# Kernel optimization log

Hardware: AMD Instinct MI355X
Metric: run time of the kernel (lower is better)

The kernel has to match this reference:

```python
import jax, jax.numpy as jnp
import numpy as np

B, T, D, EXP, K = 4, 2048, 1024, 2, 4
H = D * EXP


def setup_inputs() -> dict:
    key = jax.random.key(0)
    ks = jax.random.split(key, 8)
    x = jax.random.normal(ks[0], (B, T, D), jnp.float32)
    W_in = jax.random.normal(ks[1], (2 * H, D), jnp.float32) * D ** -0.5
    s_conv = 1.0 / np.sqrt(K)  # fan_in = (in_ch/groups)*K = K
    W_conv = jax.random.uniform(ks[2], (H, 1, K), jnp.float32, -s_conv, s_conv)
    b_conv = jax.random.uniform(ks[3], (H,), jnp.float32, -s_conv, s_conv)
    W_gates = jax.random.normal(ks[4], (3 * H, H), jnp.float32) * H ** -0.5
    s_g = 1.0 / np.sqrt(H)
    b_gates = jax.random.uniform(ks[5], (3 * H,), jnp.float32, -s_g, s_g)
    W_out = jax.random.normal(ks[6], (D, H), jnp.float32) * H ** -0.5
    alpha_p = jnp.asarray(1.0, jnp.float32)
    return {"x": x, "W_in": W_in, "W_conv": W_conv, "b_conv": b_conv,
            "W_gates": W_gates, "b_gates": b_gates, "W_out": W_out,
            "alpha_p": alpha_p}


def _scan_combine(c1, c2):
    a1, b1 = c1
    a2, b2 = c2
    return (a1 * a2, a2 * b1 + b2)


def reference(x, W_in, W_conv, b_conv, W_gates, b_gates, W_out, alpha_p):
    # input projection -> gate branch and conv branch, each [B,T,H]
    gi = jnp.einsum('btd,ed->bte', x, W_in)
    gate, u = jnp.split(gi, 2, axis=-1)
    # causal depthwise conv over time (torch pads K-1 both sides then keeps [:T])
    uc = jnp.transpose(u, (0, 2, 1))  # [B,H,T]
    v = jax.lax.conv_general_dilated(
        uc, W_conv, window_strides=(1,), padding=[(K - 1, 0)],
        dimension_numbers=('NCH', 'OIH', 'NCH'), feature_group_count=H)
    v = jnp.transpose(v + b_conv[None, :, None], (0, 2, 1))  # [B,T,H]
    # gates
    g = jnp.einsum('bth,gh->btg', v, W_gates) + b_gates
    f, i, o = jnp.split(g, 3, axis=-1)
    # reversed_sigmoid=True: alpha = sigmoid(-f) ** relu(alpha_p)
    alpha = jax.nn.sigmoid(-f) ** jax.nn.relu(alpha_p)
    xin = jax.nn.sigmoid(i) * v
    # diagonal linear recurrence h_t = alpha_t * h_{t-1} + xin_t via parallel scan
    _, h = jax.lax.associative_scan(_scan_combine, (alpha, xin), axis=1)
    h = jax.nn.sigmoid(o) * h
    return jnp.einsum('bth,dh->btd', jax.nn.gelu(gate, approximate=False) * h, W_out)
```

## Files before the change

### kernel.cpp

```cpp
#include <hip/hip_runtime.h>
#include <hip/hip_bf16.h>
#include <cstdint>
#include <cstddef>

#define B_ 4
#define T_ 2048
#define D_ 1024
#define H_ 2048

typedef __attribute__((ext_vector_type(8))) short s8v;
typedef __attribute__((ext_vector_type(4))) float f4v;

__device__ __forceinline__ float bflo(unsigned int u){ union{unsigned int i;float f;}c; c.i=u<<16; return c.f; }
__device__ __forceinline__ float bfhi(unsigned int u){ union{unsigned int i;float f;}c; c.i=u&0xffff0000u; return c.f; }
__device__ __forceinline__ unsigned short f2bf(float f){
    __hip_bfloat16 h = __float2bfloat16(f);
    union { __hip_bfloat16 h; unsigned short u; } c; c.h = h; return c.u;
}
__device__ __forceinline__ unsigned int pk2(float lo, float hi){
    return (unsigned int)f2bf(lo) | ((unsigned int)f2bf(hi) << 16);
}
__device__ __forceinline__ float sigm(float x){ return 1.f/(1.f+expf(-x)); }

__device__ __forceinline__ void gload16(const void* g, void* l){
    __builtin_amdgcn_global_load_lds(
        (const __attribute__((address_space(1))) unsigned int*)g,
        (__attribute__((address_space(3))) unsigned int*)l, 16, 0, 0);
}

__global__ __launch_bounds__(256)
void cvt8(const float* __restrict__ s, unsigned short* __restrict__ d)
{
    size_t i = ((size_t)blockIdx.x*256 + threadIdx.x)*8;
    float4 a = *(const float4*)(s+i), b = *(const float4*)(s+i+4);
    uint4 o; o.x=pk2(a.x,a.y); o.y=pk2(a.z,a.w); o.z=pk2(b.x,b.y); o.w=pk2(b.z,b.w);
    *(uint4*)(d+i)=o;
}

template<int EPI>
__global__ __launch_bounds__(512)
void mgemm256(const unsigned short* __restrict__ A, int lda,
              const unsigned short* __restrict__ Bw, int K, int N,
              const float* __restrict__ bias,
              unsigned short* __restrict__ C0, unsigned short* __restrict__ C1,
              unsigned short* __restrict__ C2,
              const unsigned short* __restrict__ vsrc, const float* __restrict__ app)
{
    __shared__ unsigned short As[2][256*64];
    __shared__ unsigned short Bs[2][256*64];
    const int tid = threadIdx.x;
    const int lane = tid & 63;
    const int wid = tid >> 6;
    const int wm = wid >> 2;
    const int wn = wid & 3;

    const int nxb = N >> 8;
    const int nwg = nxb * 32;
    const int orig = blockIdx.x;
    const int q = nwg >> 3;
    const int wg = (orig & 7) * q + (orig >> 3);
    const int m0 = (wg & 31) * 256;
    const int n0 = (wg >> 5) * 256;

    const int srow_in8 = lane >> 3;
    const int sslot    = (lane & 7) ^ srow_in8;
    const int NT = K >> 6;

    const int fr = lane & 15, fg = lane >> 4;
    const int sw = fr & 7;
    int aoff[8][2], boff[4][2];
#pragma unroll
    for (int m = 0; m < 8; ++m) {
        int row = wm*128 + m*16 + fr;
#pragma unroll
        for (int s = 0; s < 2; ++s)
            aoff[m][s] = row*128 + (((s*4 + fg) ^ sw) * 16);
    }
#pragma unroll
    for (int n = 0; n < 4; ++n) {
        int row = wn*64 + n*16 + fr;
#pragma unroll
        for (int s = 0; s < 2; ++s)
            boff[n][s] = row*128 + (((s*4 + fg) ^ sw) * 16);
    }

    f4v acc[8][4];
#pragma unroll
    for (int m = 0; m < 8; ++m)
#pragma unroll
        for (int n = 0; n < 4; ++n) { f4v z4 = {0.f,0.f,0.f,0.f}; acc[m][n] = z4; }

    auto stageA = [&](int pp, int kt) {
#pragma unroll
        for (int c = 0; c < 4; ++c) {
            int row = c*64 + wid*8 + srow_in8;
            gload16(A + (size_t)(m0 + row)*lda + kt*64 + sslot*8,
                    (void*)&As[pp][(c*64 + wid*8) * 64]);
        }
    };
    auto stageB = [&](int pp, int kt) {
#pragma unroll
        for (int c = 0; c < 4; ++c) {
            int row = c*64 + wid*8 + srow_in8;
            gload16(Bw + (size_t)(n0 + row)*K + kt*64 + sslot*8,
                    (void*)&Bs[pp][(c*64 + wid*8) * 64]);
        }
    };

    stageA(0, 0);
    stageB(0, 0);
    __syncthreads();

    for (int t = 0; t < NT; ++t) {
        const int p = t & 1;
        const char* Asb = (const char*)&As[p][0];
        const char* Bsb = (const char*)&Bs[p][0];
        const bool more = (t + 1 < NT);
#pragma unroll
        for (int ph = 0; ph < 4; ++ph) {
            const int mh = ph >> 1, nh = ph & 1;
            s8v a[4][2], b[2][2];
#pragma unroll
            for (int mi = 0; mi < 4; ++mi)
#pragma unroll
                for (int s = 0; s < 2; ++s)
                    a[mi][s] = *(const s8v*)(Asb + aoff[mh*4 + mi][s]);
#pragma unroll
            for (int ni = 0; ni < 2; ++ni)
#pragma unroll
                for (int s = 0; s < 2; ++s)
                    b[ni][s] = *(const s8v*)(Bsb + boff[nh*2 + ni][s]);
            if (ph == 0 && more) stageA(p ^ 1, t + 1);
            if (ph == 1 && more) stageB(p ^ 1, t + 1);
            __builtin_amdgcn_s_setprio(1);
#pragma unroll
            for (int mi = 0; mi < 4; ++mi)
#pragma unroll
                for (int ni = 0; ni < 2; ++ni)
#pragma unroll
                    for (int s = 0; s < 2; ++s)
                        acc[mh*4+mi][nh*2+ni] = __builtin_amdgcn_mfma_f32_16x16x32_bf16(
                            a[mi][s], b[ni][s], acc[mh*4+mi][nh*2+ni], 0, 0, 0);
            __builtin_amdgcn_s_setprio(0);
        }
        __syncthreads();
    }

    float apv = 1.f; bool ap1 = true;
    if (EPI == 2) { apv = fmaxf(app[0], 0.f); ap1 = (apv == 1.0f); }
    const int cr = (lane >> 4) * 4;
    const int cc = lane & 15;
#pragma unroll
    for (int m = 0; m < 8; ++m) {
        const int grow0 = m0 + wm*128 + m*16 + cr;
#pragma unroll
        for (int n = 0; n < 4; ++n) {
            const int colb = n0 + wn*64 + n*16;
            const int gcol = colb + cc;
            if (EPI == 1) {
                unsigned short* dst = (colb < H_) ? C0 : C1;
                const int pc = gcol & (H_-1);
#pragma unroll
                for (int j = 0; j < 4; ++j)
                    dst[(size_t)(grow0+j)*H_ + pc] = f2bf(acc[m][n][j]);
            } else {
                const int plane = colb >> 11;
                const int pc = gcol & (H_-1);
#pragma unroll
                for (int j = 0; j < 4; ++j) {
                    float val = acc[m][n][j] + bias[gcol];
                    const size_t off = (size_t)(grow0+j)*H_ + pc;
                    if (plane == 0) {
                        float s = 1.f/(1.f+expf(val));
                        C0[off] = f2bf(ap1 ? s : powf(s, apv));
                    } else if (plane == 1) {
                        C1[off] = f2bf(sigm(val) * bflo(vsrc[off]));
                    } else {
                        C2[off] = f2bf(sigm(val));
                    }
                }
            }
        }
    }
}

template<int AM, int BM, int EPI>
__global__ __launch_bounds__(256)
void mgemm(const void* __restrict__ Asrc, int lda,
           const void* __restrict__ Bsrc, int K, int N,
           const float* __restrict__ bias,
           unsigned short* __restrict__ C0, unsigned short* __restrict__ C1,
           unsigned short* __restrict__ C2, float* __restrict__ Cf,
           const unsigned short* __restrict__ vsrc, const float* __restrict__ app)
{
    __shared__ unsigned short As[128*64];
    __shared__ unsigned short Bs[128*64];
    const int tid = threadIdx.x;
    const int lane = tid & 63;
    const int wid = tid >> 6;

    const int nwg = gridDim.x * 64;
    const int orig = blockIdx.y * gridDim.x + blockIdx.x;
    const int q = nwg >> 3;
    const int wg = (orig & 7) * q + (orig >> 3);
    const int m0 = (wg & 63) * 128;
    const int n0 = (wg >> 6) * 128;

    const int ar0 = wid * 32;
    const int alr = lane >> 3;
    const int alj = lane & 7;
    const int rr = tid >> 1;
    const int kh = tid & 1;

    const int wm = wid >> 1, wn = wid & 1;
    const int fr = lane & 15, fg = lane >> 4;
    int aoff[4][2], boff[4][2];
#pragma unroll
    for (int m = 0; m < 4; ++m) {
        int row = wm*64 + m*16 + fr;
#pragma unroll
        for (int s = 0; s < 2; ++s)
            aoff[m][s] = row*128 + (((s*4 + fg) ^ (row & 7)) * 16);
    }
#pragma unroll
    for (int n = 0; n < 4; ++n) {
        int row = wn*64 + n*16 + fr;
#pragma unroll
        for (int s = 0; s < 2; ++s)
            boff[n][s] = row*128 + (((s*4 + fg) ^ (row & 7)) * 16);
    }
    const char* Asc = (const char*)As;
    const char* Bsc = (const char*)Bs;

    f4v acc[4][4];
#pragma unroll
    for (int m = 0; m < 4; ++m)
#pragma unroll
        for (int n = 0; n < 4; ++n) { f4v z4 = {0.f,0.f,0.f,0.f}; acc[m][n] = z4; }

    for (int k0 = 0; k0 < K; k0 += 64) {
        if (AM == 1) {
            const unsigned short* Ab = (const unsigned short*)Asrc;
#pragma unroll
            for (int i = 0; i < 4; ++i) {
                int row = ar0 + i*8 + alr;
                int ss = alj ^ alr;
                const char* g = (const char*)(Ab + (size_t)(m0+row)*lda + k0) + ss*16;
                gload16(g, (void*)((char*)As + (ar0 + i*8)*128));
            }
        } else {
            const float* src = (const float*)Asrc + (size_t)(m0+rr)*lda + k0 + kh*32;
            float4 v[8];
#pragma unroll
            for (int i = 0; i < 8; ++i) v[i] = ((const float4*)src)[i];
#pragma unroll
            for (int qd = 0; qd < 4; ++qd) {
                uint4 w;
                w.x = pk2(v[2*qd].x, v[2*qd].y);   w.y = pk2(v[2*qd].z, v[2*qd].w);
                w.z = pk2(v[2*qd+1].x, v[2*qd+1].y); w.w = pk2(v[2*qd+1].z, v[2*qd+1].w);
                int j = (kh*4 + qd) ^ (rr & 7);
                *(uint4*)((char*)As + rr*128 + j*16) = w;
            }
        }
        if (BM == 1) {
            const unsigned short* Bb = (const unsigned short*)Bsrc;
#pragma unroll
            for (int i = 0; i < 4; ++i) {
                int row = ar0 + i*8 + alr;
                int ss = alj ^ alr;
                const char* g = (const char*)(Bb + (size_t)(n0+row)*K + k0) + ss*16;
                gload16(g, (void*)((char*)Bs + (ar0 + i*8)*128));
            }
        } else {
            const float* src = (const float*)Bsrc + (size_t)(n0+rr)*K + k0 + kh*32;
            float4 v[8];
#pragma unroll
            for (int i = 0; i < 8; ++i) v[i] = ((const float4*)src)[i];
#pragma unroll
            for (int qd = 0; qd < 4; ++qd) {
                uint4 w;
                w.x = pk2(v[2*qd].x, v[2*qd].y);   w.y = pk2(v[2*qd].z, v[2*qd].w);
                w.z = pk2(v[2*qd+1].x, v[2*qd+1].y); w.w = pk2(v[2*qd+1].z, v[2*qd+1].w);
                int j = (kh*4 + qd) ^ (rr & 7);
                *(uint4*)((char*)Bs + rr*128 + j*16) = w;
            }
        }
        __syncthreads();
#pragma unroll
        for (int s = 0; s < 2; ++s) {
            s8v a[4], b[4];
#pragma unroll
            for (int m = 0; m < 4; ++m) a[m] = *(const s8v*)(Asc + aoff[m][s]);
#pragma unroll
            for (int n = 0; n < 4; ++n) b[n] = *(const s8v*)(Bsc + boff[n][s]);
#pragma unroll
            for (int m = 0; m < 4; ++m)
#pragma unroll
                for (int n = 0; n < 4; ++n)
                    acc[m][n] = __builtin_amdgcn_mfma_f32_16x16x32_bf16(a[m], b[n], acc[m][n], 0, 0, 0);
        }
        __syncthreads();
    }

    float apv = 1.f; bool ap1 = true;
    if (EPI == 2) { apv = fmaxf(app[0], 0.f); ap1 = (apv == 1.0f); }
    const int cr = (lane >> 4) * 4;
    const int cc = lane & 15;
#pragma unroll
    for (int m = 0; m < 4; ++m) {
        const int grow0 = m0 + wm*64 + m*16 + cr;
#pragma unroll
        for (int n = 0; n < 4; ++n) {
            const int colb = n0 + wn*64 + n*16;
            const int gcol = colb + cc;
            if (EPI == 0) {
#pragma unroll
                for (int j = 0; j < 4; ++j)
                    Cf[(size_t)(grow0+j)*N + gcol] = acc[m][n][j];
            } else if (EPI == 1) {
                unsigned short* dst = (colb < H_) ? C0 : C1;
                const int pc = gcol & (H_-1);
#pragma unroll
                for (int j = 0; j < 4; ++j)
                    dst[(size_t)(grow0+j)*H_ + pc] = f2bf(acc[m][n][j]);
            } else {
                const int plane = colb >> 11;
                const int pc = gcol & (H_-1);
#pragma unroll
                for (int j = 0; j < 4; ++j) {
                    float val = acc[m][n][j] + bias[gcol];
                    const size_t off = (size_t)(grow0+j)*H_ + pc;
                    if (plane == 0) {
                        float s = 1.f/(1.f+expf(val));
                        C0[off] = f2bf(ap1 ? s : powf(s, apv));
                    } else if (plane == 1) {
                        C1[off] = f2bf(sigm(val) * bflo(vsrc[off]));
                    } else {
                        C2[off] = f2bf(sigm(val));
                    }
                }
            }
        }
    }
}

__global__ __launch_bounds__(256)
void conv8(const unsigned short* __restrict__ u, const float* __restrict__ Wc,
           const float* __restrict__ bc, unsigned short* __restrict__ v)
{
    size_t i8 = ((size_t)blockIdx.x*256 + threadIdx.x) * 8;
    int h = (int)(i8 % H_);
    size_t bt = i8 / H_;
    int t = (int)(bt % T_);
    float w[8][4], acc[8];
#pragma unroll
    for (int j = 0; j < 8; ++j) {
        float4 wr = *(const float4*)(Wc + (h+j)*4);
        w[j][0]=wr.x; w[j][1]=wr.y; w[j][2]=wr.z; w[j][3]=wr.w;
        acc[j] = bc[h+j];
    }
    const unsigned short* up = u + bt*H_ + h;
#pragma unroll
    for (int k = 0; k < 4; ++k) {
        int dt = 3 - k;
        if (t >= dt) {
            uint4 r = *(const uint4*)(up - (size_t)dt*H_);
            float e[8] = {bflo(r.x),bfhi(r.x),bflo(r.y),bfhi(r.y),
                          bflo(r.z),bfhi(r.z),bflo(r.w),bfhi(r.w)};
#pragma unroll
            for (int j = 0; j < 8; ++j) acc[j] = fmaf(e[j], w[j][k], acc[j]);
        }
    }
    uint4 o;
    o.x = pk2(acc[0],acc[1]); o.y = pk2(acc[2],acc[3]);
    o.z = pk2(acc[4],acc[5]); o.w = pk2(acc[6],acc[7]);
    *(uint4*)(v + i8) = o;
}

__global__ __launch_bounds__(256)
void scan_chunk8(const unsigned short* __restrict__ al, const unsigned short* __restrict__ xi,
                 float* __restrict__ cA, float* __restrict__ cB, int CT)
{
    int hh = threadIdx.x * 8;
    int c = blockIdx.y, b = blockIdx.z;
    size_t base = ((size_t)b*T_ + (size_t)c*CT)*H_ + hh;
    float A[8], Bv[8];
#pragma unroll
    for (int j=0;j<8;++j){ A[j]=1.f; Bv[j]=0.f; }
    for (int t = 0; t < CT; ++t) {
        uint4 wa = *(const uint4*)(al+base);
        uint4 wx = *(const uint4*)(xi+base);
        float a[8]={bflo(wa.x),bfhi(wa.x),bflo(wa.y),bfhi(wa.y),bflo(wa.z),bfhi(wa.z),bflo(wa.w),bfhi(wa.w)};
        float x[8]={bflo(wx.x),bfhi(wx.x),bflo(wx.y),bfhi(wx.y),bflo(wx.z),bfhi(wx.z),bflo(wx.w),bfhi(wx.w)};
#pragma unroll
        for (int j=0;j<8;++j){ A[j]*=a[j]; Bv[j]=fmaf(a[j],Bv[j],x[j]); }
        base += H_;
    }
    size_t ci = ((size_t)b*gridDim.y + c)*H_ + hh;
    *(float4*)(cA+ci)   = (float4){A[0],A[1],A[2],A[3]};
    *(float4*)(cA+ci+4) = (float4){A[4],A[5],A[6],A[7]};
    *(float4*)(cB+ci)   = (float4){Bv[0],Bv[1],Bv[2],Bv[3]};
    *(float4*)(cB+ci+4) = (float4){Bv[4],Bv[5],Bv[6],Bv[7]};
}

__global__ __launch_bounds__(256)
void scan_carry8(const float* __restrict__ cA, const float* __restrict__ cB,
                 float* __restrict__ cin, int NC)
{
    int gt = blockIdx.x*256 + threadIdx.x;
    int hh = (gt * 8) % H_;
    int b  = (gt * 8) / H_;
    float h[8];
#pragma unroll
    for (int j=0;j<8;++j) h[j]=0.f;
    for (int c = 0; c < NC; ++c) {
        size_t ci = ((size_t)b*NC + c)*H_ + hh;
        *(float4*)(cin+ci)   = (float4){h[0],h[1],h[2],h[3]};
        *(float4*)(cin+ci+4) = (float4){h[4],h[5],h[6],h[7]};
        float4 a0 = *(const float4*)(cA+ci), a1 = *(const float4*)(cA+ci+4);
        float4 b0 = *(const float4*)(cB+ci), b1 = *(const float4*)(cB+ci+4);
        float a[8]={a0.x,a0.y,a0.z,a0.w,a1.x,a1.y,a1.z,a1.w};
        float x[8]={b0.x,b0.y,b0.z,b0.w,b1.x,b1.y,b1.z,b1.w};
#pragma unroll
        for (int j=0;j<8;++j) h[j] = fmaf(a[j], h[j], x[j]);
    }
}

__global__ __launch_bounds__(256)
void scan_apply8(const unsigned short* __restrict__ al, const unsigned short* __restrict__ xi,
                 const unsigned short* __restrict__ so, const unsigned short* __restrict__ ga,
                 const float* __restrict__ cin, unsigned short* __restrict__ z, int CT)
{
    int hh = threadIdx.x * 8;
    int c = blockIdx.y, b = blockIdx.z;
    size_t base = ((size_t)b*T_ + (size_t)c*CT)*H_ + hh;
    size_t ci = ((size_t)b*gridDim.y + c)*H_ + hh;
    float h[8];
    {
        float4 h0 = *(const float4*)(cin+ci), h1 = *(const float4*)(cin+ci+4);
        h[0]=h0.x; h[1]=h0.y; h[2]=h0.z; h[3]=h0.w;
        h[4]=h1.x; h[5]=h1.y; h[6]=h1.z; h[7]=h1.w;
    }
    for (int t = 0; t < CT; ++t) {
        uint4 wa = *(const uint4*)(al+base);
        uint4 wx = *(const uint4*)(xi+base);
        uint4 ws_ = *(const uint4*)(so+base);
        uint4 wg = *(const uint4*)(ga+base);
        float a[8]={bflo(wa.x),bfhi(wa.x),bflo(wa.y),bfhi(wa.y),bflo(wa.z),bfhi(wa.z),bflo(wa.w),bfhi(wa.w)};
        float x[8]={bflo(wx.x),bfhi(wx.x),bflo(wx.y),bfhi(wx.y),bflo(wx.z),bfhi(wx.z),bflo(wx.w),bfhi(wx.w)};
        float s[8]={bflo(ws_.x),bfhi(ws_.x),bflo(ws_.y),bfhi(ws_.y),bflo(ws_.z),bfhi(ws_.z),bflo(ws_.w),bfhi(ws_.w)};
        float g[8]={bflo(wg.x),bfhi(wg.x),bflo(wg.y),bfhi(wg.y),bflo(wg.z),bfhi(wg.z),bflo(wg.w),bfhi(wg.w)};
        float zo[8];
#pragma unroll
        for (int j=0;j<8;++j) {
            h[j] = fmaf(a[j], h[j], x[j]);
            float ge = 0.5f*g[j]*(1.f+erff(g[j]*0.70710678118654752f));
            zo[j] = ge * s[j] * h[j];
        }
        uint4 o;
        o.x = pk2(zo[0],zo[1]); o.y = pk2(zo[2],zo[3]);
        o.z = pk2(zo[4],zo[5]); o.w = pk2(zo[6],zo[7]);
        *(uint4*)(z + base) = o;
        base += H_;
    }
}

__global__ void zero_out(float* __restrict__ out, size_t n)
{
    for (size_t i = (size_t)blockIdx.x*256 + threadIdx.x; i < n; i += (size_t)gridDim.x*256)
        out[i] = 0.f;
}

extern "C" void kernel_launch(void* const* d_in, const int* in_sizes, int n_in,
                              void* d_out, int out_size, void* d_ws, size_t ws_size,
                              hipStream_t stream)
{
    const float* x       = (const float*)d_in[0];
    const float* W_in    = (const float*)d_in[1];
    const float* W_conv  = (const float*)d_in[2];
    const float* b_conv  = (const float*)d_in[3];
    const float* W_gates = (const float*)d_in[4];
    const float* b_gates = (const float*)d_in[5];
    const float* W_out   = (const float*)d_in[6];
    const float* alpha_p = (const float*)d_in[7];
    float* out = (float*)d_out;

    const size_t plane = (size_t)B_ * T_ * H_;
    unsigned short* gate = (unsigned short*)d_ws;
    unsigned short* u    = gate + plane;
    unsigned short* v    = u + plane;
    unsigned short* xin  = v + plane;
    unsigned short* so   = xin + plane;
    char* R = (char*)(so + plane);

    const size_t x_elems  = (size_t)B_*T_*D_;
    const size_t wg_elems = (size_t)3*H_*H_;
    const size_t wi_elems = (size_t)2*H_*D_;
    const size_t wo_elems = (size_t)D_*H_;
    const int NCF = 64;
    const size_t carry_b = 3*(size_t)B_*NCF*H_*4;
    const size_t Rneed = x_elems*2 > carry_b + wo_elems*2 ? x_elems*2 : carry_b + wo_elems*2;
    const size_t need_fast = 5*plane*2 + Rneed;

    if (ws_size >= need_fast && (size_t)out_size*4 >= (wg_elems + wi_elems)*2) {
        unsigned short* wgb  = (unsigned short*)d_out;
        unsigned short* winb = wgb + wg_elems;
        unsigned short* xb   = (unsigned short*)R;
        float* cAp  = (float*)R;
        float* cBp  = cAp + (size_t)B_*NCF*H_;
        float* cinp = cBp + (size_t)B_*NCF*H_;
        unsigned short* woutb = (unsigned short*)(cinp + (size_t)B_*NCF*H_);
        const int CT = T_ / NCF;

        cvt8<<<(unsigned)(x_elems/2048),  256, 0, stream>>>(x, xb);
        cvt8<<<(unsigned)(wi_elems/2048), 256, 0, stream>>>(W_in, winb);
        cvt8<<<(unsigned)(wg_elems/2048), 256, 0, stream>>>(W_gates, wgb);
        mgemm256<1><<<dim3(16*32), 512, 0, stream>>>(
            xb, D_, winb, D_, 2*H_, nullptr, gate, u, nullptr, nullptr, nullptr);
        conv8<<<(unsigned)(plane/8/256), 256, 0, stream>>>(u, W_conv, b_conv, v);
        cvt8<<<(unsigned)(wo_elems/2048), 256, 0, stream>>>(W_out, woutb);
        mgemm256<2><<<dim3(24*32), 512, 0, stream>>>(
            v, H_, wgb, H_, 3*H_, b_gates, u, xin, so, v, alpha_p);
        scan_chunk8<<<dim3(1,NCF,B_), 256, 0, stream>>>(u, xin, cAp, cBp, CT);
        scan_carry8<<<(B_*H_/8)/256, 256, 0, stream>>>(cAp, cBp, cinp, NCF);
        scan_apply8<<<dim3(1,NCF,B_), 256, 0, stream>>>(u, xin, so, gate, cinp, v, CT);
        mgemm<1,1,0><<<dim3(8,64), 256, 0, stream>>>(
            v, H_, woutb, H_, D_, nullptr, nullptr, nullptr, nullptr, out, nullptr, nullptr);
        return;
    }

    float* cAp = (float*)R;
    int NC = 64;
    if (ws_size < 5*plane*2 + 3*(size_t)B_*64*H_*4) {
        NC = 16;
        if (ws_size < 5*plane*2 + 3*(size_t)B_*16*H_*4) {
            zero_out<<<2048, 256, 0, stream>>>(out, (size_t)out_size);
            return;
        }
    }
    const int CT = T_ / NC;
    float* cBp  = cAp + (size_t)B_*NC*H_;
    float* cinp = cBp + (size_t)B_*NC*H_;

    mgemm<0,0,1><<<dim3(32,64), 256, 0, stream>>>(
        x, D_, W_in, D_, 2*H_, nullptr, gate, u, nullptr, nullptr, nullptr, nullptr);
    conv8<<<(unsigned)(plane/8/256), 256, 0, stream>>>(u, W_conv, b_conv, v);
    mgemm<1,0,2><<<dim3(48,64), 256, 0, stream>>>(
        v, H_, W_gates, H_, 3*H_, b_gates, u, xin, so, nullptr, v, alpha_p);
    scan_chunk8<<<dim3(1,NC,B_), 256, 0, stream>>>(u, xin, cAp, cBp, CT);
    scan_carry8<<<(B_*H_/8)/256, 256, 0, stream>>>(cAp, cBp, cinp, NC);
    scan_apply8<<<dim3(1,NC,B_), 256, 0, stream>>>(u, xin, so, gate, cinp, v, CT);
    mgemm<1,0,0><<<dim3(8,64), 256, 0, stream>>>(
        v, H_, W_out, H_, D_, nullptr, nullptr, nullptr, nullptr, out, nullptr, nullptr);
}
```

Measured before the change: 643.3 us.

## Rework 256x256 GEMM into 4-stage K=32 pipeline with one barrier per step

Replaces the double-buffered K=64 tile GEMM with a four-deep ring of K=32 LDS tiles. Tiles are prefetched three steps ahead, and explicit vmcnt waits plus a single barrier per iteration replace the per-phase staging and __syncthreads. The LDS layout and swizzle change to pack row pairs, and launch bounds now request two blocks per CU. The goal is to hide global-load latency better and cut synchronisation. The trade-off is more loop iterations with less MFMA work each, plus hand-tuned waitcnt logic that is fragile.

```diff
diff --git a/kernel.cpp b/kernel.cpp
--- a/kernel.cpp
+++ b/kernel.cpp
@@ -38,50 +38,57 @@
 }
 
 template<int EPI>
-__global__ __launch_bounds__(512)
-void mgemm256(const unsigned short* __restrict__ A, int lda,
-              const unsigned short* __restrict__ Bw, int K, int N,
-              const float* __restrict__ bias,
-              unsigned short* __restrict__ C0, unsigned short* __restrict__ C1,
-              unsigned short* __restrict__ C2,
-              const unsigned short* __restrict__ vsrc, const float* __restrict__ app)
-{
-    __shared__ unsigned short As[2][256*64];
-    __shared__ unsigned short Bs[2][256*64];
+__global__ __launch_bounds__(512, 2)
+void pgemm(const unsigned short* __restrict__ A, int lda,
+           const unsigned short* __restrict__ Bw, int K, int N,
+           const float* __restrict__ bias,
+           unsigned short* __restrict__ C0, unsigned short* __restrict__ C1,
+           unsigned short* __restrict__ C2,
+           const unsigned short* __restrict__ vsrc, const float* __restrict__ app)
+{
+    __shared__ unsigned short lds[4][16384];
     const int tid = threadIdx.x;
     const int lane = tid & 63;
     const int wid = tid >> 6;
     const int wm = wid >> 2;
     const int wn = wid & 3;
 
-    const int nxb = N >> 8;
-    const int nwg = nxb * 32;
+    const int nwg = (N >> 8) * 32;
     const int orig = blockIdx.x;
     const int q = nwg >> 3;
     const int wg = (orig & 7) * q + (orig >> 3);
     const int m0 = (wg & 31) * 256;
     const int n0 = (wg >> 5) * 256;
 
-    const int srow_in8 = lane >> 3;
-    const int sslot    = (lane & 7) ^ srow_in8;
-    const int NT = K >> 6;
+    const char* srcA[2]; const char* srcB[2];
+    int dstOff[2];
+#pragma unroll
+    for (int r = 0; r < 2; ++r) {
+        int si = r*512 + tid;
+        int rp = si >> 3;
+        int sl = (si & 7) ^ (rp & 7);
+        int row = 2*rp + (sl >> 2);
+        int fg  = sl & 3;
+        srcA[r] = (const char*)(A  + (size_t)(m0 + row) * lda + fg*8);
+        srcB[r] = (const char*)(Bw + (size_t)(n0 + row) * K   + fg*8);
+        dstOff[r] = (r*512 + wid*64) * 16;
+    }
 
     const int fr = lane & 15, fg = lane >> 4;
-    const int sw = fr & 7;
-    int aoff[8][2], boff[4][2];
+    int aoff[8], boff[4];
 #pragma unroll
     for (int m = 0; m < 8; ++m) {
         int row = wm*128 + m*16 + fr;
-#pragma unroll
-        for (int s = 0; s < 2; ++s)
-            aoff[m][s] = row*128 + (((s*4 + fg) ^ sw) * 16);
+        int rp = row >> 1;
+        int sl = ((row & 1)*4 + fg) ^ (rp & 7);
+        aoff[m] = rp*128 + sl*16;
     }
 #pragma unroll
     for (int n = 0; n < 4; ++n) {
         int row = wn*64 + n*16 + fr;
-#pragma unroll
-        for (int s = 0; s < 2; ++s)
-            boff[n][s] = row*128 + (((s*4 + fg) ^ sw) * 16);
+        int rp = row >> 1;
+        int sl = ((row & 1)*4 + fg) ^ (rp & 7);
+        boff[n] = 16384 + rp*128 + sl*16;
     }
 
     f4v acc[8][4];
@@ -90,60 +97,43 @@
 #pragma unroll
         for (int n = 0; n < 4; ++n) { f4v z4 = {0.f,0.f,0.f,0.f}; acc[m][n] = z4; }
 
-    auto stageA = [&](int pp, int kt) {
-#pragma unroll
-        for (int c = 0; c < 4; ++c) {
-            int row = c*64 + wid*8 + srow_in8;
-            gload16(A + (size_t)(m0 + row)*lda + kt*64 + sslot*8,
-                    (void*)&As[pp][(c*64 + wid*8) * 64]);
-        }
+    const int NT = K >> 5;
+    auto stage = [&](int t) {
+        char* base = (char*)&lds[t & 3][0];
+        const size_t ko = (size_t)t * 64;
+#pragma unroll
+        for (int r = 0; r < 2; ++r) gload16(srcA[r] + ko, base + dstOff[r]);
+#pragma unroll
+        for (int r = 0; r < 2; ++r) gload16(srcB[r] + ko, base + 16384 + dstOff[r]);
     };
-    auto stageB = [&](int pp, int kt) {
-#pragma unroll
-        for (int c = 0; c < 4; ++c) {
-            int row = c*64 + wid*8 + srow_in8;
-            gload16(Bw + (size_t)(n0 + row)*K + kt*64 + sslot*8,
-                    (void*)&Bs[pp][(c*64 + wid*8) * 64]);
-        }
-    };
-
-    stageA(0, 0);
-    stageB(0, 0);
-    __syncthreads();
+
+    stage(0); stage(1); stage(2);
+    asm volatile("s_waitcnt vmcnt(8)" ::: "memory");
+    __builtin_amdgcn_s_barrier();
+    __builtin_amdgcn_sched_barrier(0);
 
     for (int t = 0; t < NT; ++t) {
-        const int p = t & 1;
-        const char* Asb = (const char*)&As[p][0];
-        const char* Bsb = (const char*)&Bs[p][0];
-        const bool more = (t + 1 < NT);
-#pragma unroll
-        for (int ph = 0; ph < 4; ++ph) {
-            const int mh = ph >> 1, nh = ph & 1;
-            s8v a[4][2], b[2][2];
-#pragma unroll
-            for (int mi = 0; mi < 4; ++mi)
-#pragma unroll
-                for (int s = 0; s < 2; ++s)
-                    a[mi][s] = *(const s8v*)(Asb + aoff[mh*4 + mi][s]);
-#pragma unroll
-            for (int ni = 0; ni < 2; ++ni)
-#pragma unroll
-                for (int s = 0; s < 2; ++s)
-                    b[ni][s] = *(const s8v*)(Bsb + boff[nh*2 + ni][s]);
-            if (ph == 0 && more) stageA(p ^ 1, t + 1);
-            if (ph == 1 && more) stageB(p ^ 1, t + 1);
-            __builtin_amdgcn_s_setprio(1);
-#pragma unroll
-            for (int mi = 0; mi < 4; ++mi)
-#pragma unroll
-                for (int ni = 0; ni < 2; ++ni)
-#pragma unroll
-                    for (int s = 0; s < 2; ++s)
-                        acc[mh*4+mi][nh*2+ni] = __builtin_amdgcn_mfma_f32_16x16x32_bf16(
-                            a[mi][s], b[ni][s], acc[mh*4+mi][nh*2+ni], 0, 0, 0);
-            __builtin_amdgcn_s_setprio(0);
-        }
-        __syncthreads();
+        const char* buf = (const char*)&lds[t & 3][0];
+        if (t + 3 < NT) stage(t + 3);
+        s8v a[8], b[4];
+#pragma unroll
+        for (int m = 0; m < 8; ++m) a[m] = *(const s8v*)(buf + aoff[m]);
+#pragma unroll
+        for (int n = 0; n < 4; ++n) b[n] = *(const s8v*)(buf + boff[n]);
+        __builtin_amdgcn_s_setprio(1);
+#pragma unroll
+        for (int m = 0; m < 8; ++m)
+#pragma unroll
+            for (int n = 0; n < 4; ++n)
+                acc[m][n] = __builtin_amdgcn_mfma_f32_16x16x32_bf16(a[m], b[n], acc[m][n], 0, 0, 0);
+        __builtin_amdgcn_s_setprio(0);
+        if (t + 3 < NT)       { asm volatile("s_waitcnt vmcnt(8)" ::: "memory"); }
+        else if (t + 3 == NT) { asm volatile("s_waitcnt vmcnt(4)" ::: "memory"); }
+        else if (t + 2 == NT) { asm volatile("s_waitcnt vmcnt(0)" ::: "memory"); }
+        if (t + 1 < NT) {
+            __builtin_amdgcn_s_barrier();
+            __builtin_amdgcn_sched_barrier(0);
+        }
     }
 
     float apv = 1.f; bool ap1 = true;
@@ -515,11 +505,11 @@
         cvt8<<<(unsigned)(x_elems/2048),  256, 0, stream>>>(x, xb);
         cvt8<<<(unsigned)(wi_elems/2048), 256, 0, stream>>>(W_in, winb);
         cvt8<<<(unsigned)(wg_elems/2048), 256, 0, stream>>>(W_gates, wgb);
-        mgemm256<1><<<dim3(16*32), 512, 0, stream>>>(
+        pgemm<1><<<dim3(512), 512, 0, stream>>>(
             xb, D_, winb, D_, 2*H_, nullptr, gate, u, nullptr, nullptr, nullptr);
         conv8<<<(unsigned)(plane/8/256), 256, 0, stream>>>(u, W_conv, b_conv, v);
         cvt8<<<(unsigned)(wo_elems/2048), 256, 0, stream>>>(W_out, woutb);
-        mgemm256<2><<<dim3(24*32), 512, 0, stream>>>(
+        pgemm<2><<<dim3(768), 512, 0, stream>>>(
             v, H_, wgb, H_, 3*H_, b_gates, u, xin, so, v, alpha_p);
         scan_chunk8<<<dim3(1,NCF,B_), 256, 0, stream>>>(u, xin, cAp, cBp, CT);
         scan_carry8<<<(B_*H_/8)/256, 256, 0, stream>>>(cAp, cBp, cinp, NCF);
```

New measurement: 648.0 us. No clear change (+0.7%).
